# Kernel optimization log

Measured on AMD Instinct MI355X. Metric: run time of the kernel, lower is better.

## Reference

```python
import jax, jax.numpy as jnp
import numpy as np

B, S, N_STATE, N_HEAD = 8, 4096, 1024, 16
H_DIM = N_STATE // N_HEAD           # 64
NUM_ROT = H_DIM // 2                # 32
BASE = 10000.0


def setup_inputs() -> dict:
    key = jax.random.key(0)
    k0, k1, k2 = jax.random.split(key, 3)
    x = jax.random.normal(k0, (B, S, N_STATE), dtype=jnp.float32)
    thetas = 0.1 * jax.random.normal(k1, (NUM_ROT,), dtype=jnp.float32)
    rotation_pairs = jax.random.uniform(k2, (NUM_ROT, 2), dtype=jnp.float32) * H_DIM
    theta_scale = jnp.ones((1,), dtype=jnp.float32)
    # orthogonal init, mirroring reset_parameters()
    q, _ = np.linalg.qr(np.random.RandomState(0).randn(H_DIM, H_DIM))
    rotation_matrix = jnp.asarray(q, dtype=jnp.float32)
    inv_freq = 1.0 / (BASE ** (jnp.arange(0, H_DIM, 2, dtype=jnp.float32) / H_DIM))
    return {"x": x, "thetas": thetas, "rotation_pairs": rotation_pairs,
            "theta_scale": theta_scale, "rotation_matrix": rotation_matrix,
            "inv_freq": inv_freq}


def reference(x, thetas, rotation_pairs, theta_scale, rotation_matrix, inv_freq):
    b, s, n_state = x.shape
    h_dim = rotation_matrix.shape[0]
    n_head = n_state // h_dim

    # rotation_pairs[k].long() in torch -> truncation toward zero (values >= 0)
    idx = rotation_pairs.astype(jnp.int32)

    # Compose all Givens rotations into one h_dim x h_dim matrix (tiny),
    # instead of num_rotations full matmuls against x.
    # math.cos/math.sin in the torch code detach theta -> stop_gradient.
    thetas_scaled = jax.lax.stop_gradient(thetas * theta_scale[0])

    def step(R, inputs):
        i, j, theta = inputs
        c, sn = jnp.cos(theta), jnp.sin(theta)
        G = jnp.eye(h_dim, dtype=x.dtype)
        # same assignment order as torch (handles i == j overwrite identically)
        G = G.at[i, i].set(c).at[i, j].set(-sn).at[j, i].set(sn).at[j, j].set(c)
        return R @ G, None

    R, _ = jax.lax.scan(step, jnp.eye(h_dim, dtype=x.dtype),
                        (idx[:, 0], idx[:, 1], thetas_scaled))
    M = R @ rotation_matrix                       # [h_dim, h_dim]

    xh = x.reshape(b, s, n_head, h_dim)
    xr = jnp.einsum('bshd,de->bshe', xh, M)       # learned rotation

    pos = jnp.arange(s, dtype=x.dtype)            # [s]
    sinusoid = pos[:, None] * inv_freq[None, :]   # [s, h_dim//2]
    sin = jnp.sin(sinusoid)[None, :, None, :]
    cos = jnp.cos(sinusoid)[None, :, None, :]

    x1, x2 = xr[..., 0::2], xr[..., 1::2]
    out = jnp.concatenate([x1 * cos - x2 * sin, x1 * sin + x2 * cos], axis=-1)
    return out.reshape(b, s, n_state)
```

## Files before the change

### kernel.cpp

```cpp
#include <hip/hip_runtime.h>

#define S_      4096
#define NROT    32
#define NCHUNK  32768
#define NBLK    2048
#define WPB     4
#define NWAVE   (NBLK * WPB)
#define NITER   (NCHUNK / NWAVE)

typedef __bf16 bf16x4 __attribute__((ext_vector_type(4)));
typedef __bf16 bf16x8 __attribute__((ext_vector_type(8)));
typedef float  f32x4  __attribute__((ext_vector_type(4)));
typedef unsigned short ushort_t;

__device__ __forceinline__ int swzb(int a) { return a ^ (((a >> 7) & 7) << 4); }

union Scratch {
    float    M[64][64];
    ushort_t frag[4096];
    float    chunk[WPB][512];
};

__global__ __launch_bounds__(256) void rope_fused_kernel(
    const float* __restrict__ x,
    const float* __restrict__ thetas,
    const float* __restrict__ rot_pairs,
    const float* __restrict__ theta_scale,
    const float* __restrict__ rot_matrix,
    const float* __restrict__ inv_freq,
    float* __restrict__ out)
{
    __shared__ __align__(16) Scratch sc;
    __shared__ float trig[NROT][2];

    const int t    = threadIdx.x;
    const int lane = t & 63;
    const int w    = t >> 6;
    const int l15  = lane & 15;
    const int lhi  = lane >> 4;
    const int u    = l15 >> 1;
    const bool even = (lane & 1) == 0;

    const int c0 = blockIdx.x * WPB + w;

    f32x4 qa[4], qb[4];
    {
        const float* xa = x + (size_t)c0 * 1024 + lane * 4;
        #pragma unroll
        for (int k = 0; k < 4; ++k)
            qa[k] = *reinterpret_cast<const f32x4*>(xa + k * 256);
    }

    {
        const int row = t >> 2, c4 = (t & 3) * 16;
        const float* src = rot_matrix + row * 64 + c4;
        #pragma unroll
        for (int j = 0; j < 4; ++j)
            *reinterpret_cast<f32x4*>(&sc.M[row][c4 + 4 * j]) =
                *reinterpret_cast<const f32x4*>(src + 4 * j);
    }
    if (t < NROT) {
        const float th = thetas[t] * theta_scale[0];
        trig[t][0] = cosf(th);
        trig[t][1] = sinf(th);
    }
    __syncthreads();

    if (t < 64) {
        #pragma unroll
        for (int k = NROT - 1; k >= 0; --k) {
            const int   i = (int)rot_pairs[2 * k];
            const int   j = (int)rot_pairs[2 * k + 1];
            const float c = trig[k][0];
            const float s = trig[k][1];
            const float mi = sc.M[i][t];
            const float mj = sc.M[j][t];
            if (i == j) {
                sc.M[i][t] = c * mi;
            } else {
                sc.M[i][t] = fmaf(c, mi, -s * mj);
                sc.M[j][t] = fmaf(s, mi,  c * mj);
            }
        }
    }
    __syncthreads();

    float vals[16];
    #pragma unroll
    for (int m = 0; m < 16; ++m) {
        const int F  = t * 16 + m;
        const int f  = F >> 9;
        const int ln = (F >> 3) & 63;
        const int i  = F & 7;
        const int kt = f >> 2, nt = f & 3;
        const int d  = kt * 32 + 8 * (ln >> 4) + i;
        const int n  = ln & 15;
        const int e  = 8 * (n >> 1) + 2 * nt + (n & 1);
        vals[m] = sc.M[d][e];
    }
    __syncthreads();

    {
        uint32_t dw[8];
        #pragma unroll
        for (int m = 0; m < 8; ++m) {
            union { __bf16 h; ushort_t s; } lo, hi;
            lo.h = (__bf16)vals[2 * m];
            hi.h = (__bf16)vals[2 * m + 1];
            dw[m] = (uint32_t)lo.s | ((uint32_t)hi.s << 16);
        }
        uint32_t* dst = reinterpret_cast<uint32_t*>(sc.frag + t * 16);
        *reinterpret_cast<uint4*>(dst)     = make_uint4(dw[0], dw[1], dw[2], dw[3]);
        *reinterpret_cast<uint4*>(dst + 4) = make_uint4(dw[4], dw[5], dw[6], dw[7]);
    }
    __syncthreads();

    bf16x8 bf[2][4];
    #pragma unroll
    for (int kt = 0; kt < 2; ++kt)
        #pragma unroll
        for (int nt = 0; nt < 4; ++nt)
            bf[kt][nt] = *reinterpret_cast<const bf16x8*>(
                sc.frag + ((kt * 4 + nt) * 512 + lane * 8));
    __syncthreads();

    {
        const float* xb = x + (size_t)(c0 + NWAVE) * 1024 + lane * 4;
        #pragma unroll
        for (int k = 0; k < 4; ++k)
            qb[k] = *reinterpret_cast<const f32x4*>(xb + k * 256);
    }

    const f32x4 invf = *reinterpret_cast<const f32x4*>(inv_freq + 4 * u);
    const float INV2PI = 0.15915494309189535f;
    char* wbuf = reinterpret_cast<char*>(sc.chunk[w]);

    int wr_off[4];
    #pragma unroll
    for (int k = 0; k < 4; ++k)
        wr_off[k] = swzb((k * 4 + lhi) * 128 + l15 * 8);
    const int rd0 = swzb(l15 * 128 + lhi * 16);
    const int rd1 = swzb(l15 * 128 + lhi * 16 + 64);

    int c = c0;
    #pragma unroll 1
    for (int p = 0; p < NITER / 2; ++p) {
        const bool pref = (p + 1 < NITER / 2);
        #pragma unroll
        for (int half = 0; half < 2; ++half) {
            f32x4* q = half ? qb : qa;
            const int cc = c + half * NWAVE;

            #pragma unroll
            for (int k = 0; k < 4; ++k) {
                bf16x4 h;
                #pragma unroll
                for (int i = 0; i < 4; ++i) h[i] = (__bf16)q[k][i];
                *reinterpret_cast<bf16x4*>(wbuf + wr_off[k]) = h;
            }

            if (pref) {
                const float* xn = x + (size_t)(cc + 2 * NWAVE) * 1024 + lane * 4;
                #pragma unroll
                for (int k = 0; k < 4; ++k)
                    q[k] = *reinterpret_cast<const f32x4*>(xn + k * 256);
            }

            const bf16x8 a0 = *reinterpret_cast<const bf16x8*>(wbuf + rd0);
            const bf16x8 a1 = *reinterpret_cast<const bf16x8*>(wbuf + rd1);

            f32x4 acc[4];
            #pragma unroll
            for (int nt = 0; nt < 4; ++nt) {
                acc[nt] = (f32x4){0.f, 0.f, 0.f, 0.f};
                acc[nt] = __builtin_amdgcn_mfma_f32_16x16x32_bf16(a0, bf[0][nt], acc[nt], 0, 0, 0);
                acc[nt] = __builtin_amdgcn_mfma_f32_16x16x32_bf16(a1, bf[1][nt], acc[nt], 0, 0, 0);
            }

            const int s = cc & (S_ - 1);
            float cs[4], sn2[4];
            #pragma unroll
            for (int nt = 0; nt < 4; ++nt) {
                float rev = (float)s * invf[nt] * INV2PI;
                rev -= floorf(rev);
                const float sv = __builtin_amdgcn_sinf(rev);
                cs[nt]  = __builtin_amdgcn_cosf(rev);
                sn2[nt] = even ? -sv : sv;
            }

            float* outc = out + (size_t)cc * 1024;
            #pragma unroll
            for (int j = 0; j < 4; ++j) {
                f32x4 res;
                #pragma unroll
                for (int nt = 0; nt < 4; ++nt) {
                    const float own = acc[nt][j];
                    const float oth = __shfl_xor(own, 1, 64);
                    res[nt] = fmaf(oth, sn2[nt], own * cs[nt]);
                }
                const int row  = lhi * 4 + j;
                const int col0 = (even ? 0 : 32) + 4 * u;
                __builtin_nontemporal_store(
                    res, reinterpret_cast<f32x4*>(outc + row * 64 + col0));
            }
        }
        c += 2 * NWAVE;
    }
}

extern "C" void kernel_launch(void* const* d_in, const int* in_sizes, int n_in,
                              void* d_out, int out_size, void* d_ws, size_t ws_size,
                              hipStream_t stream)
{
    const float* x           = (const float*)d_in[0];
    const float* thetas      = (const float*)d_in[1];
    const float* rot_pairs   = (const float*)d_in[2];
    const float* theta_scale = (const float*)d_in[3];
    const float* rot_matrix  = (const float*)d_in[4];
    const float* inv_freq    = (const float*)d_in[5];
    float*       outp        = (float*)d_out;

    rope_fused_kernel<<<NBLK, 256, 0, stream>>>(
        x, thetas, rot_pairs, theta_scale, rot_matrix, inv_freq, outp);
}
```

Measured before the change: 50.26 us.

## Use single-buffer prefetch, pad M stride, and raise occupancy via launch bounds

Replaces the two-chunk register double buffer with a single prefetched chunk per iteration, halving the x registers held in flight. It adds a minimum-blocks hint of 8 to launch_bounds to push for higher occupancy. It also pads the shared M matrix row stride to 68 to cut LDS bank conflicts during the column-wise rotation updates and the fragment gather. The trade-off is less memory-level parallelism per wave in exchange for more resident waves; the padding also grows shared memory slightly.

```diff
diff --git a/kernel.cpp b/kernel.cpp
--- a/kernel.cpp
+++ b/kernel.cpp
@@ -7,6 +7,7 @@
 #define WPB     4
 #define NWAVE   (NBLK * WPB)
 #define NITER   (NCHUNK / NWAVE)
+#define MST     68
 
 typedef __bf16 bf16x4 __attribute__((ext_vector_type(4)));
 typedef __bf16 bf16x8 __attribute__((ext_vector_type(8)));
@@ -16,12 +17,12 @@
 __device__ __forceinline__ int swzb(int a) { return a ^ (((a >> 7) & 7) << 4); }
 
 union Scratch {
-    float    M[64][64];
+    float    M[64][MST];
     ushort_t frag[4096];
     float    chunk[WPB][512];
 };
 
-__global__ __launch_bounds__(256) void rope_fused_kernel(
+__global__ __launch_bounds__(256, 8) void rope_fused_kernel(
     const float* __restrict__ x,
     const float* __restrict__ thetas,
     const float* __restrict__ rot_pairs,
@@ -43,12 +44,12 @@
 
     const int c0 = blockIdx.x * WPB + w;
 
-    f32x4 qa[4], qb[4];
+    f32x4 q[4];
     {
         const float* xa = x + (size_t)c0 * 1024 + lane * 4;
         #pragma unroll
         for (int k = 0; k < 4; ++k)
-            qa[k] = *reinterpret_cast<const f32x4*>(xa + k * 256);
+            q[k] = *reinterpret_cast<const f32x4*>(xa + k * 256);
     }
 
     {
@@ -124,13 +125,6 @@
                 sc.frag + ((kt * 4 + nt) * 512 + lane * 8));
     __syncthreads();
 
-    {
-        const float* xb = x + (size_t)(c0 + NWAVE) * 1024 + lane * 4;
-        #pragma unroll
-        for (int k = 0; k < 4; ++k)
-            qb[k] = *reinterpret_cast<const f32x4*>(xb + k * 256);
-    }
-
     const f32x4 invf = *reinterpret_cast<const f32x4*>(inv_freq + 4 * u);
     const float INV2PI = 0.15915494309189535f;
     char* wbuf = reinterpret_cast<char*>(sc.chunk[w]);
@@ -144,67 +138,61 @@
 
     int c = c0;
     #pragma unroll 1
-    for (int p = 0; p < NITER / 2; ++p) {
-        const bool pref = (p + 1 < NITER / 2);
-        #pragma unroll
-        for (int half = 0; half < 2; ++half) {
-            f32x4* q = half ? qb : qa;
-            const int cc = c + half * NWAVE;
-
+    for (int it = 0; it < NITER; ++it) {
+        #pragma unroll
+        for (int k = 0; k < 4; ++k) {
+            bf16x4 h;
             #pragma unroll
-            for (int k = 0; k < 4; ++k) {
-                bf16x4 h;
-                #pragma unroll
-                for (int i = 0; i < 4; ++i) h[i] = (__bf16)q[k][i];
-                *reinterpret_cast<bf16x4*>(wbuf + wr_off[k]) = h;
-            }
-
-            if (pref) {
-                const float* xn = x + (size_t)(cc + 2 * NWAVE) * 1024 + lane * 4;
-                #pragma unroll
-                for (int k = 0; k < 4; ++k)
-                    q[k] = *reinterpret_cast<const f32x4*>(xn + k * 256);
-            }
-
-            const bf16x8 a0 = *reinterpret_cast<const bf16x8*>(wbuf + rd0);
-            const bf16x8 a1 = *reinterpret_cast<const bf16x8*>(wbuf + rd1);
-
-            f32x4 acc[4];
+            for (int i = 0; i < 4; ++i) h[i] = (__bf16)q[k][i];
+            *reinterpret_cast<bf16x4*>(wbuf + wr_off[k]) = h;
+        }
+
+        if (it + 1 < NITER) {
+            const float* xn = x + (size_t)(c + NWAVE) * 1024 + lane * 4;
+            #pragma unroll
+            for (int k = 0; k < 4; ++k)
+                q[k] = *reinterpret_cast<const f32x4*>(xn + k * 256);
+        }
+
+        const bf16x8 a0 = *reinterpret_cast<const bf16x8*>(wbuf + rd0);
+        const bf16x8 a1 = *reinterpret_cast<const bf16x8*>(wbuf + rd1);
+
+        f32x4 acc[4];
+        #pragma unroll
+        for (int nt = 0; nt < 4; ++nt) {
+            acc[nt] = (f32x4){0.f, 0.f, 0.f, 0.f};
+            acc[nt] = __builtin_amdgcn_mfma_f32_16x16x32_bf16(a0, bf[0][nt], acc[nt], 0, 0, 0);
+            acc[nt] = __builtin_amdgcn_mfma_f32_16x16x32_bf16(a1, bf[1][nt], acc[nt], 0, 0, 0);
+        }
+
+        const int s = c & (S_ - 1);
+        float cs[4], sn2[4];
+        #pragma unroll
+        for (int nt = 0; nt < 4; ++nt) {
+            float rev = (float)s * invf[nt] * INV2PI;
+            rev -= floorf(rev);
+            const float sv = __builtin_amdgcn_sinf(rev);
+            cs[nt]  = __builtin_amdgcn_cosf(rev);
+            sn2[nt] = even ? -sv : sv;
+        }
+
+        float* outc = out + (size_t)c * 1024;
+        #pragma unroll
+        for (int j = 0; j < 4; ++j) {
+            f32x4 res;
             #pragma unroll
             for (int nt = 0; nt < 4; ++nt) {
-                acc[nt] = (f32x4){0.f, 0.f, 0.f, 0.f};
-                acc[nt] = __builtin_amdgcn_mfma_f32_16x16x32_bf16(a0, bf[0][nt], acc[nt], 0, 0, 0);
-                acc[nt] = __builtin_amdgcn_mfma_f32_16x16x32_bf16(a1, bf[1][nt], acc[nt], 0, 0, 0);
+                const float own = acc[nt][j];
+                const float oth = __shfl_xor(own, 1, 64);
+                res[nt] = fmaf(oth, sn2[nt], own * cs[nt]);
             }
-
-            const int s = cc & (S_ - 1);
-            float cs[4], sn2[4];
-            #pragma unroll
-            for (int nt = 0; nt < 4; ++nt) {
-                float rev = (float)s * invf[nt] * INV2PI;
-                rev -= floorf(rev);
-                const float sv = __builtin_amdgcn_sinf(rev);
-                cs[nt]  = __builtin_amdgcn_cosf(rev);
-                sn2[nt] = even ? -sv : sv;
-            }
-
-            float* outc = out + (size_t)cc * 1024;
-            #pragma unroll
-            for (int j = 0; j < 4; ++j) {
-                f32x4 res;
-                #pragma unroll
-                for (int nt = 0; nt < 4; ++nt) {
-                    const float own = acc[nt][j];
-                    const float oth = __shfl_xor(own, 1, 64);
-                    res[nt] = fmaf(oth, sn2[nt], own * cs[nt]);
-                }
-                const int row  = lhi * 4 + j;
-                const int col0 = (even ? 0 : 32) + 4 * u;
-                __builtin_nontemporal_store(
-                    res, reinterpret_cast<f32x4*>(outc + row * 64 + col0));
-            }
-        }
-        c += 2 * NWAVE;
+            const int row  = lhi * 4 + j;
+            const int col0 = (even ? 0 : 32) + 4 * u;
+            __builtin_nontemporal_store(
+                res, reinterpret_cast<f32x4*>(outc + row * 64 + col0));
+        }
+
+        c += NWAVE;
     }
 }
 
```

Measured after the change: 107.0 us. 113% more time.
